# Performance work log

Hardware: AMD Instinct MI355X
Metric: run time of the kernel (lower is better)

Reference implementation:

```python
import jax, jax.numpy as jnp
import numpy as np

N_WIRES = 12
N_QLAYERS = 2
DIM = 2 ** N_WIRES


def setup_inputs() -> dict:
    key = jax.random.key(0)
    k0, k1, k2, k3 = jax.random.split(key, 4)
    x = jax.random.normal(k0, (2048, 1024), dtype=jnp.float32)
    # TT cores: ranks [1,16,1], input dims [32,32], output dims [8,9]
    core0 = jax.random.normal(k1, (1, 32, 8, 16), dtype=jnp.float32) * 0.05
    core1 = jax.random.normal(k2, (16, 32, 9, 1), dtype=jnp.float32) * 0.05
    tt_bias = jnp.zeros((72,), dtype=jnp.float32)
    global_angles = jax.random.normal(k3, (N_QLAYERS, N_WIRES, 3), dtype=jnp.float32) * 0.1
    return {"x": x, "core0": core0, "core1": core1, "tt_bias": tt_bias,
            "global_angles": global_angles}


def _rot(angles):
    # angles [..., 3] -> combined U = Rz @ Ry @ Rx, shape [..., 2, 2] complex64
    half = angles * 0.5
    cx, sx = jnp.cos(half[..., 0]), jnp.sin(half[..., 0])
    cy, sy = jnp.cos(half[..., 1]), jnp.sin(half[..., 1])
    cz, sz = jnp.cos(half[..., 2]), jnp.sin(half[..., 2])
    zero = jnp.zeros_like(cx)
    cplx = jax.lax.complex
    Rx = jnp.stack([jnp.stack([cplx(cx, zero), cplx(zero, -sx)], -1),
                    jnp.stack([cplx(zero, -sx), cplx(cx, zero)], -1)], -2)
    Ry = jnp.stack([jnp.stack([cplx(cy, zero), cplx(-sy, zero)], -1),
                    jnp.stack([cplx(sy, zero), cplx(cy, zero)], -1)], -2)
    ez, ezc = cplx(cz, -sz), cplx(cz, sz)  # exp(-i z/2), exp(+i z/2)
    zc = cplx(zero, zero)
    Rz = jnp.stack([jnp.stack([ez, zc], -1), jnp.stack([zc, ezc], -1)], -2)
    return jnp.einsum('...ij,...jk,...kl->...il', Rz, Ry, Rx)


def _apply_1q(state, U, w):
    # state [bsz, 2^n]; U [bsz, 2, 2]; wire 0 = most significant qubit
    bsz = state.shape[0]
    left, right = 2 ** w, 2 ** (N_WIRES - w - 1)
    s = state.reshape(bsz, left, 2, right)
    s = jnp.einsum('bij,bljr->blir', U, s)
    return s.reshape(bsz, DIM)


def _cnot(state, c, t):
    bsz = state.shape[0]
    s = state.reshape((bsz,) + (2,) * N_WIRES)
    s0 = jax.lax.index_in_dim(s, 0, c + 1, keepdims=True)
    s1 = jax.lax.index_in_dim(s, 1, c + 1, keepdims=True)
    s1 = jnp.flip(s1, axis=t + 1)  # flip target amplitudes where control = 1
    return jnp.concatenate([s0, s1], axis=c + 1).reshape(bsz, DIM)


def reference(x, core0, core1, tt_bias, global_angles):
    bsz = x.shape[0]
    # --- TT layer: x[b,32,32] contracted with two TT cores -> [b,8,9] -> [b,72]
    x_rs = x.reshape(bsz, 32, 32)
    tt_out = jnp.einsum('bij,aipq,qjrs->bpr', x_rs, core0, core1).reshape(bsz, -1) + tt_bias
    # residual global angles
    angles = global_angles[None, :, :, :] + tt_out.reshape(bsz, N_QLAYERS, N_WIRES, 3)
    U = _rot(angles)  # [bsz, L, n, 2, 2]
    # --- tensor-product Ry encoding of x[:, :n_wires] on |0...0>
    enc = x[:, :N_WIRES] * 0.5
    amp = jnp.stack([jnp.cos(enc), jnp.sin(enc)], -1)  # [bsz, n, 2]
    state = amp[:, 0, :]
    for w in range(1, N_WIRES):
        state = (state[:, :, None] * amp[:, w, None, :]).reshape(bsz, -1)
    state = state.astype(jnp.complex64)  # [bsz, 2^n]
    # --- VQC layers: fused Rz@Ry@Rx per wire, then ring CNOT (noise_prob=0)
    for k in range(N_QLAYERS):
        for w in range(N_WIRES):
            state = _apply_1q(state, U[:, k, w], w)
        for i in range(N_WIRES - 1):
            state = _cnot(state, i, i + 1)
        state = _cnot(state, N_WIRES - 1, 0)
    # --- MeasureAll(PauliZ): <Z_w> per wire
    probs = jnp.real(state * jnp.conj(state))  # [bsz, 2^n]
    idx = jnp.arange(DIM)[:, None]
    bits = (idx >> jnp.arange(N_WIRES - 1, -1, -1)[None, :]) & 1  # [2^n, n]
    zsign = (1.0 - 2.0 * bits).astype(jnp.float32)
    return probs @ zsign  # [bsz, n_wires]
```

## Files before the change

### kernel.cpp

```cpp
#include <hip/hip_runtime.h>
#include <math.h>

#define N_WIRES 12

__host__ __device__ constexpr int parity12(int x) {
  x ^= x >> 8; x ^= x >> 4; x ^= x >> 2; x ^= x >> 1;
  return x & 1;
}

typedef float2 f2;
__device__ __forceinline__ f2 mk2(float a, float b) { f2 r; r.x = a; r.y = b; return r; }
__device__ __forceinline__ f2 pkmul(f2 a, f2 b) {
  f2 d; asm("v_pk_mul_f32 %0, %1, %2" : "=v"(d) : "v"(a), "v"(b)); return d;
}
__device__ __forceinline__ f2 pkfma(f2 a, f2 b, f2 c) {
  f2 d; asm("v_pk_fma_f32 %0, %1, %2, %3" : "=v"(d) : "v"(a), "v"(b), "v"(c)); return d;
}
__device__ __forceinline__ f2 shfl_xor2(f2 v, int m) {
  f2 r; r.x = __shfl_xor(v.x, m, 64); r.y = __shfl_xor(v.y, m, 64); return r;
}
__device__ __forceinline__ f2 swap2(f2 v) { return mk2(v.y, v.x); }

__global__ __launch_bounds__(256) void build_w_kernel(
    const float* __restrict__ core0,
    const float* __restrict__ core1,
    float* __restrict__ Wt) {
  int idx = blockIdx.x * 256 + threadIdx.x;
  int k = idx / 72;
  int o = idx - k * 72;
  int i = k >> 5, jj = k & 31;
  int p = o / 9, r = o - p * 9;
  float acc = 0.f;
#pragma unroll
  for (int q = 0; q < 16; ++q) {
    acc += core0[(i * 8 + p) * 16 + q] * core1[(q * 32 + jj) * 9 + r];
  }
  int og = o / 9, j = o - og * 9;
  Wt[k * 96 + og * 12 + j] = acc;
}

__global__ __launch_bounds__(512) void tt_gemm2(
    const float* __restrict__ x,
    const float* __restrict__ Wt,
    const float* __restrict__ bias,
    float* __restrict__ ttout) {
  __shared__ __align__(16) float ws[128 * 96];
  __shared__ __align__(16) float xs[8 * 132];
  __shared__ float part[16 * 8 * 73];
  const int t = threadIdx.x;
  const int row0 = blockIdx.x * 8;
  const int kk = t >> 5;
  const int rp = (t >> 3) & 3;
  const int og = t & 7;
  const int r0 = rp * 2;

  float a0[9], a1[9];
#pragma unroll
  for (int j = 0; j < 9; ++j) { a0[j] = 0.f; a1[j] = 0.f; }

  for (int s = 0; s < 8; ++s) {
    __syncthreads();
    const float4* Wg = (const float4*)(Wt + s * 128 * 96);
#pragma unroll
    for (int i = 0; i < 6; ++i) {
      const int idx = i * 512 + t;
      ((float4*)ws)[idx] = Wg[idx];
    }
    if (t < 256) {
      const int rr = t >> 5, j4 = t & 31;
      *(float4*)&xs[rr * 132 + j4 * 4] =
          *(const float4*)(x + (size_t)(row0 + rr) * 1024 + s * 128 + j4 * 4);
    }
    __syncthreads();
#pragma unroll
    for (int i = 0; i < 8; ++i) {
      const int k = kk + i * 16;
      const float4 wA = *(const float4*)&ws[k * 96 + og * 12];
      const float4 wB = *(const float4*)&ws[k * 96 + og * 12 + 4];
      const float w8 = ws[k * 96 + og * 12 + 8];
      const float x0v = xs[r0 * 132 + k];
      const float x1v = xs[r0 * 132 + 132 + k];
      a0[0] += x0v * wA.x; a0[1] += x0v * wA.y;
      a0[2] += x0v * wA.z; a0[3] += x0v * wA.w;
      a0[4] += x0v * wB.x; a0[5] += x0v * wB.y;
      a0[6] += x0v * wB.z; a0[7] += x0v * wB.w;
      a0[8] += x0v * w8;
      a1[0] += x1v * wA.x; a1[1] += x1v * wA.y;
      a1[2] += x1v * wA.z; a1[3] += x1v * wA.w;
      a1[4] += x1v * wB.x; a1[5] += x1v * wB.y;
      a1[6] += x1v * wB.z; a1[7] += x1v * wB.w;
      a1[8] += x1v * w8;
    }
  }

#pragma unroll
  for (int j = 0; j < 9; ++j) {
    part[(kk * 8 + r0) * 73 + og * 9 + j] = a0[j];
    part[(kk * 8 + r0 + 1) * 73 + og * 9 + j] = a1[j];
  }
  __syncthreads();

  for (int i = t; i < 576; i += 512) {
    const int r = i / 72, o = i - r * 72;
    float ssum = bias[o];
#pragma unroll
    for (int kq = 0; kq < 16; ++kq) ssum += part[(kq * 8 + r) * 73 + o];
    ttout[(size_t)(row0 + r) * 72 + o] = ssum;
  }
}

template <int MASK, int ROW>
__device__ __forceinline__ void gate_pk(f2 R[8], f2 I[8],
    float u00r, float u00i, float u01r, float u01i,
    f2* __restrict__ buf, int t) {
  constexpr int RM = MASK & 15;
  constexpr int TM = (MASK >> 4) & 0xFF;
  constexpr int LM = TM & 63;
  constexpr bool LDSX = (TM & 0xC0) != 0;
  constexpr int FLIP = parity12(ROW & 3);
  constexpr int JX = (RM == 0) ? 0 : (((RM & 1) ? (RM ^ 3) : RM) >> 1);
  constexpr bool SW = (RM & 1) != 0;

  const int tsgn = (__popc(ROW & (t << 4)) & 1) << 31;
  const float dEi = __int_as_float(__float_as_int(u00i) ^ tsgn);
  const float oEr = __int_as_float(__float_as_int(u01r) ^ tsgn);
  const float ndEi = -dEi, noEr = -oEr;
  const f2 A  = mk2(u00r, u00r);
  const f2 C  = mk2(u01i, u01i);
  const f2 nC = mk2(-u01i, -u01i);

  auto Dof = [&](int pe, int ph) { return mk2(pe ? ndEi : dEi, ph ? ndEi : dEi); };
  auto Oof = [&](int pe, int ph) { return mk2(pe ? noEr : oEr, ph ? noEr : oEr); };

  auto upd = [&](int j, f2 Rb, f2 Ib, f2& outR, f2& outI) {
    const int pe = parity12(ROW & (2 * j));
    const int ph = pe ^ FLIP;
    const f2 Dj = Dof(pe, ph), nDj = Dof(!pe, !ph), Oj = Oof(pe, ph);
    const f2 a = R[j], ii = I[j];
    outR = pkfma(A, a, pkfma(nDj, ii, pkfma(Oj, Rb, pkmul(nC, Ib))));
    outI = pkfma(Dj, a, pkfma(A, ii, pkfma(C, Rb, pkmul(Oj, Ib))));
  };

  if constexpr (LDSX) {
    const int tp = t ^ TM;
#pragma unroll
    for (int ph2 = 0; ph2 < 2; ++ph2) {
      __syncthreads();
#pragma unroll
      for (int j = 0; j < 8; ++j) {
        const bool inA = (j < 2) || (j > 5);
        if ((ph2 == 0) == inA) {
          const int slot = inA ? ((j < 2) ? j : j - 4) : (j - 2);
          buf[slot * 512 + t] = R[j];
          buf[slot * 512 + 256 + t] = I[j];
        }
      }
      __syncthreads();
#pragma unroll
      for (int j = 0; j < 8; ++j) {
        const bool inA = (j < 2) || (j > 5);
        if ((ph2 == 0) == inA) {
          const int j2 = j ^ JX;
          const bool inA2 = (j2 < 2) || (j2 > 5);
          const int slot2 = inA2 ? ((j2 < 2) ? j2 : j2 - 4) : (j2 - 2);
          f2 Rb = buf[slot2 * 512 + tp];
          f2 Ib = buf[slot2 * 512 + 256 + tp];
          if constexpr (SW) { Rb = swap2(Rb); Ib = swap2(Ib); }
          upd(j, Rb, Ib, R[j], I[j]);
        }
      }
    }
  } else if constexpr (LM != 0) {
#pragma unroll
    for (int j = 0; j < 8; ++j) {
      const f2 Rb = shfl_xor2(R[j], LM);
      const f2 Ib = shfl_xor2(I[j], LM);
      upd(j, Rb, Ib, R[j], I[j]);
    }
  } else {
#pragma unroll
    for (int j = 0; j < 8; ++j) {
      const int j2 = j ^ JX;
      if (j < j2) {
        f2 Rb1 = R[j2], Ib1 = I[j2], Rb2 = R[j], Ib2 = I[j];
        if constexpr (SW) {
          Rb1 = swap2(Rb1); Ib1 = swap2(Ib1);
          Rb2 = swap2(Rb2); Ib2 = swap2(Ib2);
        }
        f2 nR1, nI1, nR2, nI2;
        upd(j, Rb1, Ib1, nR1, nI1);
        upd(j2, Rb2, Ib2, nR2, nI2);
        R[j] = nR1; I[j] = nI1; R[j2] = nR2; I[j2] = nI2;
      }
    }
  }
}

__global__ __launch_bounds__(256, 5) void vqc_kernel4(
    const float* __restrict__ x,
    const float* __restrict__ ttout,
    const float* __restrict__ gang,
    float* __restrict__ out) {
  const int b = blockIdx.x;
  const int t = threadIdx.x;

  __shared__ __align__(16) f2 buf[2048];
  __shared__ float sU[12][4];
  __shared__ float sFre[12][2], sFim[12][2];

  const float* ttb = ttout + (size_t)b * 72;

  if (t < 24) {
    const int w = (t < 12) ? t : t - 12;
    const int k = (t < 12) ? 1 : 0;
    const int gbase = (k * 12 + w) * 3;
    const int tbase = k * 36 + w * 3;
    float a0 = gang[gbase + 0] + ttb[tbase + 0];
    float a1 = gang[gbase + 1] + ttb[tbase + 1];
    float a2 = gang[gbase + 2] + ttb[tbase + 2];
    float cx = cosf(0.5f * a0), sx = sinf(0.5f * a0);
    float cy = cosf(0.5f * a1), sy = sinf(0.5f * a1);
    float cz = cosf(0.5f * a2), sz = sinf(0.5f * a2);
    float m00r = cy * cx,   m00i = sy * sx;
    float m01r = -sy * cx,  m01i = -cy * sx;
    float m10r = sy * cx,   m10i = -cy * sx;
    float m11r = cy * cx,   m11i = -sy * sx;
    float U00r = cz * m00r + sz * m00i, U00i = cz * m00i - sz * m00r;
    float U01r = cz * m01r + sz * m01i, U01i = cz * m01i - sz * m01r;
    float U10r = cz * m10r - sz * m10i, U10i = cz * m10i + sz * m10r;
    float U11r = cz * m11r - sz * m11i, U11i = cz * m11i + sz * m11r;
    if (t < 12) {
      sU[w][0] = U00r; sU[w][1] = U00i;
      sU[w][2] = U01r; sU[w][3] = U01i;
    } else {
      const float e = x[(size_t)b * 1024 + w] * 0.5f;
      const float c = cosf(e), s = sinf(e);
      sFre[w][0] = U00r * c + U01r * s;  sFim[w][0] = U00i * c + U01i * s;
      sFre[w][1] = U10r * c + U11r * s;  sFim[w][1] = U10i * c + U11i * s;
    }
  }
  __syncthreads();

  float vr[16], vi[16];
  {
    const int bits[7] = {(t >> 7) & 1,
                         ((t >> 6) ^ (t >> 5)) & 1,
                         ((t >> 5) ^ (t >> 4)) & 1,
                         ((t >> 4) ^ (t >> 3)) & 1,
                         ((t >> 3) ^ (t >> 2)) & 1,
                         ((t >> 2) ^ (t >> 1)) & 1,
                         ((t >> 1) ^ t) & 1};
    float br_ = 1.f, bi_ = 0.f;
#pragma unroll
    for (int w = 0; w < 7; ++w) {
      const float fr = sFre[w][bits[w]], fi = sFim[w][bits[w]];
      const float nr = br_ * fr - bi_ * fi;
      const float ni = br_ * fi + bi_ * fr;
      br_ = nr; bi_ = ni;
    }
    const int t0 = t & 1;
    float b7r[2], b7i[2];
#pragma unroll
    for (int r3 = 0; r3 < 2; ++r3) {
      const float fr = sFre[7][t0 ^ r3], fi = sFim[7][t0 ^ r3];
      b7r[r3] = br_ * fr - bi_ * fi;
      b7i[r3] = br_ * fi + bi_ * fr;
    }
    float hr[8], hi[8];
#pragma unroll
    for (int j = 0; j < 8; ++j) {
      const int r3 = j >> 2, r2 = (j >> 1) & 1, r1 = j & 1;
      const float ar = sFre[8][r3 ^ r2], ai = sFim[8][r3 ^ r2];
      const float cr = sFre[9][r2 ^ r1], ci = sFim[9][r2 ^ r1];
      hr[j] = ar * cr - ai * ci; hi[j] = ar * ci + ai * cr;
    }
    float gr[4], gi[4];
#pragma unroll
    for (int j = 0; j < 4; ++j) {
      const int r1 = j >> 1, r0 = j & 1;
      const float ar = sFre[10][r1 ^ r0], ai = sFim[10][r1 ^ r0];
      const float cr = sFre[11][r0], ci = sFim[11][r0];
      gr[j] = ar * cr - ai * ci; gi[j] = ar * ci + ai * cr;
    }
#pragma unroll
    for (int r = 0; r < 16; ++r) {
      const int r3 = r >> 3, hj = r >> 1, gj = r & 3;
      const float pr = hr[hj] * gr[gj] - hi[hj] * gi[gj];
      const float pi = hr[hj] * gi[gj] + hi[hj] * gr[gj];
      vr[r] = b7r[r3] * pr - b7i[r3] * pi;
      vi[r] = b7r[r3] * pi + b7i[r3] * pr;
    }
  }
  f2 R[8], I[8];
#pragma unroll
  for (int j = 0; j < 8; ++j) {
    R[j] = mk2(vr[2 * j], vr[(2 * j) ^ 3]);
    I[j] = mk2(vi[2 * j], vi[(2 * j) ^ 3]);
  }

#define GATE(MASK, ROW, GID) \
  gate_pk<MASK, ROW>(R, I, sU[GID][0], sU[GID][1], sU[GID][2], sU[GID][3], buf, t)

  GATE(0xC00, 0x400, 0);
  GATE(0x200, 0xE00, 1);
  GATE(0x100, 0xD00, 2);
  GATE(0x080, 0xC80, 3);
  GATE(0x040, 0xC40, 4);
  GATE(0x020, 0xC20, 5);
  GATE(0x010, 0xC10, 6);
  GATE(0x008, 0xC08, 7);
  GATE(0x004, 0xC04, 8);
  GATE(0x002, 0xC02, 9);
  GATE(0x001, 0xC01, 10);
  GATE(0xBFF, 0xC00, 11);
#undef GATE

  constexpr int MROWS[12] = {0xFFF, 0xA00, 0x700, 0xB80, 0x7C0, 0xBE0,
                             0x7F0, 0xBF8, 0x7FC, 0xBFE, 0x7FF, 0xBFF};
  const f2 Spp = mk2(1.f, 1.f),  Smm = mk2(-1.f, -1.f);
  const f2 Spm = mk2(1.f, -1.f), Smp = mk2(-1.f, 1.f);
  f2 acc2[12];
#pragma unroll
  for (int w = 0; w < 12; ++w) acc2[w] = mk2(0.f, 0.f);
#pragma unroll
  for (int j = 0; j < 8; ++j) {
    const f2 pr2 = pkfma(I[j], I[j], pkmul(R[j], R[j]));
#pragma unroll
    for (int w = 0; w < 12; ++w) {
      const int sl = parity12(MROWS[w] & (2 * j));
      const int sh = sl ^ parity12(MROWS[w] & 3);
      const f2 S = sl ? (sh ? Smm : Smp) : (sh ? Spm : Spp);
      acc2[w] = pkfma(S, pr2, acc2[w]);
    }
  }
  __syncthreads();
  float* rbuf = (float*)buf;
#pragma unroll
  for (int w = 0; w < 12; ++w) {
    float v = acc2[w].x + acc2[w].y;
    if (__popc(MROWS[w] & (t << 4)) & 1) v = -v;
#pragma unroll
    for (int off = 32; off > 0; off >>= 1) v += __shfl_down(v, off, 64);
    if ((t & 63) == 0) rbuf[(t >> 6) * 12 + w] = v;
  }
  __syncthreads();
  if (t < 12) {
    out[(size_t)b * 12 + t] = rbuf[t] + rbuf[12 + t] + rbuf[24 + t] + rbuf[36 + t];
  }
}

extern "C" void kernel_launch(void* const* d_in, const int* in_sizes, int n_in,
                              void* d_out, int out_size, void* d_ws, size_t ws_size,
                              hipStream_t stream) {
  const float* x       = (const float*)d_in[0];
  const float* core0   = (const float*)d_in[1];
  const float* core1   = (const float*)d_in[2];
  const float* tt_bias = (const float*)d_in[3];
  const float* gang    = (const float*)d_in[4];
  float* out = (float*)d_out;
  float* Wt     = (float*)d_ws;
  float* ttout  = (float*)d_ws + 98304;

  const int bsz = in_sizes[0] / 1024;

  build_w_kernel<<<288, 256, 0, stream>>>(core0, core1, Wt);
  tt_gemm2<<<bsz / 8, 512, 0, stream>>>(x, Wt, tt_bias, ttout);
  vqc_kernel4<<<bsz, 256, 0, stream>>>(x, ttout, gang, out);
}
```

Baseline: 58.79 us.

## Simulate each sample's statevector within a single wavefront to drop LDS exchanges

The VQC kernel now assigns one 64-lane wavefront per batch sample, with 64 amplitudes held in registers per lane (32 packed pairs), instead of one 256-thread block per sample with 16 per thread. Every gate is then done with register swaps or cross-lane shuffles, so the shared-memory exchange and __syncthreads barriers of high-wire gates go away. Unitary coefficients are broadcast with shuffles instead of LDS, and the final reduction writes straight from lane 0. The cost is about four times the register state per thread and lower occupancy (launch bounds changed from 5 to 2), plus more shuffles per gate, which risks spills and less latency hiding.

```diff
diff --git a/kernel.cpp b/kernel.cpp
--- a/kernel.cpp
+++ b/kernel.cpp
@@ -20,6 +20,11 @@
   f2 r; r.x = __shfl_xor(v.x, m, 64); r.y = __shfl_xor(v.y, m, 64); return r;
 }
 __device__ __forceinline__ f2 swap2(f2 v) { return mk2(v.y, v.x); }
+
+struct cpx { float r, i; };
+__device__ __forceinline__ cpx cmulc(cpx a, cpx b) {
+  return {a.r * b.r - a.i * b.i, a.r * b.i + a.i * b.r};
+}
 
 __global__ __launch_bounds__(256) void build_w_kernel(
     const float* __restrict__ core0,
@@ -110,18 +115,15 @@
 }
 
 template <int MASK, int ROW>
-__device__ __forceinline__ void gate_pk(f2 R[8], f2 I[8],
-    float u00r, float u00i, float u01r, float u01i,
-    f2* __restrict__ buf, int t) {
-  constexpr int RM = MASK & 15;
-  constexpr int TM = (MASK >> 4) & 0xFF;
-  constexpr int LM = TM & 63;
-  constexpr bool LDSX = (TM & 0xC0) != 0;
+__device__ __forceinline__ void gate_pk(f2 R[32], f2 I[32],
+    float u00r, float u00i, float u01r, float u01i, int lane) {
+  constexpr int RM = MASK & 0x3F;
+  constexpr int LM = (MASK >> 6) & 0x3F;
   constexpr int FLIP = parity12(ROW & 3);
   constexpr int JX = (RM == 0) ? 0 : (((RM & 1) ? (RM ^ 3) : RM) >> 1);
   constexpr bool SW = (RM & 1) != 0;
 
-  const int tsgn = (__popc(ROW & (t << 4)) & 1) << 31;
+  const int tsgn = (__popc((ROW >> 6) & lane) & 1) << 31;
   const float dEi = __int_as_float(__float_as_int(u00i) ^ tsgn);
   const float oEr = __int_as_float(__float_as_int(u01r) ^ tsgn);
   const float ndEi = -dEi, noEr = -oEr;
@@ -141,45 +143,35 @@
     outI = pkfma(Dj, a, pkfma(A, ii, pkfma(C, Rb, pkmul(Oj, Ib))));
   };
 
-  if constexpr (LDSX) {
-    const int tp = t ^ TM;
-#pragma unroll
-    for (int ph2 = 0; ph2 < 2; ++ph2) {
-      __syncthreads();
-#pragma unroll
-      for (int j = 0; j < 8; ++j) {
-        const bool inA = (j < 2) || (j > 5);
-        if ((ph2 == 0) == inA) {
-          const int slot = inA ? ((j < 2) ? j : j - 4) : (j - 2);
-          buf[slot * 512 + t] = R[j];
-          buf[slot * 512 + 256 + t] = I[j];
-        }
-      }
-      __syncthreads();
-#pragma unroll
-      for (int j = 0; j < 8; ++j) {
-        const bool inA = (j < 2) || (j > 5);
-        if ((ph2 == 0) == inA) {
-          const int j2 = j ^ JX;
-          const bool inA2 = (j2 < 2) || (j2 > 5);
-          const int slot2 = inA2 ? ((j2 < 2) ? j2 : j2 - 4) : (j2 - 2);
-          f2 Rb = buf[slot2 * 512 + tp];
-          f2 Ib = buf[slot2 * 512 + 256 + tp];
-          if constexpr (SW) { Rb = swap2(Rb); Ib = swap2(Ib); }
-          upd(j, Rb, Ib, R[j], I[j]);
-        }
-      }
-    }
-  } else if constexpr (LM != 0) {
-#pragma unroll
-    for (int j = 0; j < 8; ++j) {
+  if constexpr (LM != 0 && RM == 0) {
+#pragma unroll
+    for (int j = 0; j < 32; ++j) {
       const f2 Rb = shfl_xor2(R[j], LM);
       const f2 Ib = shfl_xor2(I[j], LM);
-      upd(j, Rb, Ib, R[j], I[j]);
+      f2 nR, nI;
+      upd(j, Rb, Ib, nR, nI);
+      R[j] = nR; I[j] = nI;
+    }
+  } else if constexpr (LM != 0 && RM != 0) {
+#pragma unroll
+    for (int j = 0; j < 32; ++j) {
+      const int j2 = j ^ JX;
+      if (j < j2) {
+        f2 Rb1 = shfl_xor2(R[j2], LM), Ib1 = shfl_xor2(I[j2], LM);
+        f2 Rb2 = shfl_xor2(R[j],  LM), Ib2 = shfl_xor2(I[j],  LM);
+        if constexpr (SW) {
+          Rb1 = swap2(Rb1); Ib1 = swap2(Ib1);
+          Rb2 = swap2(Rb2); Ib2 = swap2(Ib2);
+        }
+        f2 nR1, nI1, nR2, nI2;
+        upd(j, Rb1, Ib1, nR1, nI1);
+        upd(j2, Rb2, Ib2, nR2, nI2);
+        R[j] = nR1; I[j] = nI1; R[j2] = nR2; I[j2] = nI2;
+      }
     }
   } else {
 #pragma unroll
-    for (int j = 0; j < 8; ++j) {
+    for (int j = 0; j < 32; ++j) {
       const int j2 = j ^ JX;
       if (j < j2) {
         f2 Rb1 = R[j2], Ib1 = I[j2], Rb2 = R[j], Ib2 = I[j];
@@ -196,110 +188,121 @@
   }
 }
 
-__global__ __launch_bounds__(256, 5) void vqc_kernel4(
+__global__ __launch_bounds__(256, 2) void vqc_kernel5(
     const float* __restrict__ x,
     const float* __restrict__ ttout,
     const float* __restrict__ gang,
     float* __restrict__ out) {
-  const int b = blockIdx.x;
   const int t = threadIdx.x;
-
-  __shared__ __align__(16) f2 buf[2048];
-  __shared__ float sU[12][4];
-  __shared__ float sFre[12][2], sFim[12][2];
-
+  const int lane = t & 63;
+  const int b = blockIdx.x * 4 + (t >> 6);
   const float* ttb = ttout + (size_t)b * 72;
 
-  if (t < 24) {
-    const int w = (t < 12) ? t : t - 12;
-    const int k = (t < 12) ? 1 : 0;
+  float c0 = 0.f, c1 = 0.f, c2 = 0.f, c3 = 0.f;
+  const bool uLane = lane < 12;
+  const bool fLane = (lane >= 16) && (lane < 28);
+  if (uLane || fLane) {
+    const int w = uLane ? lane : lane - 16;
+    const int k = uLane ? 1 : 0;
     const int gbase = (k * 12 + w) * 3;
     const int tbase = k * 36 + w * 3;
-    float a0 = gang[gbase + 0] + ttb[tbase + 0];
-    float a1 = gang[gbase + 1] + ttb[tbase + 1];
-    float a2 = gang[gbase + 2] + ttb[tbase + 2];
-    float cx = cosf(0.5f * a0), sx = sinf(0.5f * a0);
-    float cy = cosf(0.5f * a1), sy = sinf(0.5f * a1);
-    float cz = cosf(0.5f * a2), sz = sinf(0.5f * a2);
-    float m00r = cy * cx,   m00i = sy * sx;
-    float m01r = -sy * cx,  m01i = -cy * sx;
-    float m10r = sy * cx,   m10i = -cy * sx;
-    float m11r = cy * cx,   m11i = -sy * sx;
-    float U00r = cz * m00r + sz * m00i, U00i = cz * m00i - sz * m00r;
-    float U01r = cz * m01r + sz * m01i, U01i = cz * m01i - sz * m01r;
-    float U10r = cz * m10r - sz * m10i, U10i = cz * m10i + sz * m10r;
-    float U11r = cz * m11r - sz * m11i, U11i = cz * m11i + sz * m11r;
-    if (t < 12) {
-      sU[w][0] = U00r; sU[w][1] = U00i;
-      sU[w][2] = U01r; sU[w][3] = U01i;
+    const float a0 = gang[gbase + 0] + ttb[tbase + 0];
+    const float a1 = gang[gbase + 1] + ttb[tbase + 1];
+    const float a2 = gang[gbase + 2] + ttb[tbase + 2];
+    const float cx = cosf(0.5f * a0), sx = sinf(0.5f * a0);
+    const float cy = cosf(0.5f * a1), sy = sinf(0.5f * a1);
+    const float cz = cosf(0.5f * a2), sz = sinf(0.5f * a2);
+    const float m00r = cy * cx,   m00i = sy * sx;
+    const float m01r = -sy * cx,  m01i = -cy * sx;
+    const float m10r = sy * cx,   m10i = -cy * sx;
+    const float m11r = cy * cx,   m11i = -sy * sx;
+    const float U00r = cz * m00r + sz * m00i, U00i = cz * m00i - sz * m00r;
+    const float U01r = cz * m01r + sz * m01i, U01i = cz * m01i - sz * m01r;
+    const float U10r = cz * m10r - sz * m10i, U10i = cz * m10i + sz * m10r;
+    const float U11r = cz * m11r - sz * m11i, U11i = cz * m11i + sz * m11r;
+    if (uLane) {
+      c0 = U00r; c1 = U00i; c2 = U01r; c3 = U01i;
     } else {
       const float e = x[(size_t)b * 1024 + w] * 0.5f;
-      const float c = cosf(e), s = sinf(e);
-      sFre[w][0] = U00r * c + U01r * s;  sFim[w][0] = U00i * c + U01i * s;
-      sFre[w][1] = U10r * c + U11r * s;  sFim[w][1] = U10i * c + U11i * s;
-    }
-  }
-  __syncthreads();
-
-  float vr[16], vi[16];
-  {
-    const int bits[7] = {(t >> 7) & 1,
-                         ((t >> 6) ^ (t >> 5)) & 1,
-                         ((t >> 5) ^ (t >> 4)) & 1,
-                         ((t >> 4) ^ (t >> 3)) & 1,
-                         ((t >> 3) ^ (t >> 2)) & 1,
-                         ((t >> 2) ^ (t >> 1)) & 1,
-                         ((t >> 1) ^ t) & 1};
-    float br_ = 1.f, bi_ = 0.f;
-#pragma unroll
-    for (int w = 0; w < 7; ++w) {
-      const float fr = sFre[w][bits[w]], fi = sFim[w][bits[w]];
-      const float nr = br_ * fr - bi_ * fi;
-      const float ni = br_ * fi + bi_ * fr;
-      br_ = nr; bi_ = ni;
-    }
-    const int t0 = t & 1;
-    float b7r[2], b7i[2];
-#pragma unroll
-    for (int r3 = 0; r3 < 2; ++r3) {
-      const float fr = sFre[7][t0 ^ r3], fi = sFim[7][t0 ^ r3];
-      b7r[r3] = br_ * fr - bi_ * fi;
-      b7i[r3] = br_ * fi + bi_ * fr;
-    }
-    float hr[8], hi[8];
-#pragma unroll
-    for (int j = 0; j < 8; ++j) {
-      const int r3 = j >> 2, r2 = (j >> 1) & 1, r1 = j & 1;
-      const float ar = sFre[8][r3 ^ r2], ai = sFim[8][r3 ^ r2];
-      const float cr = sFre[9][r2 ^ r1], ci = sFim[9][r2 ^ r1];
-      hr[j] = ar * cr - ai * ci; hi[j] = ar * ci + ai * cr;
-    }
-    float gr[4], gi[4];
-#pragma unroll
-    for (int j = 0; j < 4; ++j) {
-      const int r1 = j >> 1, r0 = j & 1;
-      const float ar = sFre[10][r1 ^ r0], ai = sFim[10][r1 ^ r0];
-      const float cr = sFre[11][r0], ci = sFim[11][r0];
-      gr[j] = ar * cr - ai * ci; gi[j] = ar * ci + ai * cr;
-    }
-#pragma unroll
-    for (int r = 0; r < 16; ++r) {
-      const int r3 = r >> 3, hj = r >> 1, gj = r & 3;
-      const float pr = hr[hj] * gr[gj] - hi[hj] * gi[gj];
-      const float pi = hr[hj] * gi[gj] + hi[hj] * gr[gj];
-      vr[r] = b7r[r3] * pr - b7i[r3] * pi;
-      vi[r] = b7r[r3] * pi + b7i[r3] * pr;
-    }
-  }
-  f2 R[8], I[8];
-#pragma unroll
-  for (int j = 0; j < 8; ++j) {
-    R[j] = mk2(vr[2 * j], vr[(2 * j) ^ 3]);
-    I[j] = mk2(vi[2 * j], vi[(2 * j) ^ 3]);
-  }
-
-#define GATE(MASK, ROW, GID) \
-  gate_pk<MASK, ROW>(R, I, sU[GID][0], sU[GID][1], sU[GID][2], sU[GID][3], buf, t)
+      const float cc = cosf(e), ss = sinf(e);
+      c0 = U00r * cc + U01r * ss;  c1 = U00i * cc + U01i * ss;
+      c2 = U10r * cc + U11r * ss;  c3 = U10i * cc + U11i * ss;
+    }
+  }
+
+  float Fr[12][2], Fi[12][2];
+#pragma unroll
+  for (int w = 0; w < 12; ++w) {
+    Fr[w][0] = __shfl(c0, 16 + w, 64);
+    Fi[w][0] = __shfl(c1, 16 + w, 64);
+    Fr[w][1] = __shfl(c2, 16 + w, 64);
+    Fi[w][1] = __shfl(c3, 16 + w, 64);
+  }
+
+  const int bw0 = (lane >> 5) & 1;
+  const int bw1 = ((lane >> 4) ^ (lane >> 3)) & 1;
+  const int bw2 = ((lane >> 3) ^ (lane >> 2)) & 1;
+  const int bw3 = ((lane >> 2) ^ (lane >> 1)) & 1;
+  const int bw4 = ((lane >> 1) ^ lane) & 1;
+  const int l0 = lane & 1;
+
+  cpx P = {bw0 ? Fr[0][1] : Fr[0][0], bw0 ? Fi[0][1] : Fi[0][0]};
+  P = cmulc(P, {bw1 ? Fr[1][1] : Fr[1][0], bw1 ? Fi[1][1] : Fi[1][0]});
+  P = cmulc(P, {bw2 ? Fr[2][1] : Fr[2][0], bw2 ? Fi[2][1] : Fi[2][0]});
+  P = cmulc(P, {bw3 ? Fr[3][1] : Fr[3][0], bw3 ? Fi[3][1] : Fi[3][0]});
+  P = cmulc(P, {bw4 ? Fr[4][1] : Fr[4][0], bw4 ? Fi[4][1] : Fi[4][0]});
+
+  cpx A1[2];
+  A1[0] = {l0 ? Fr[5][1] : Fr[5][0], l0 ? Fi[5][1] : Fi[5][0]};
+  A1[1] = {l0 ? Fr[5][0] : Fr[5][1], l0 ? Fi[5][0] : Fi[5][1]};
+  cpx A2[4];
+#pragma unroll
+  for (int a = 0; a < 2; ++a)
+#pragma unroll
+    for (int bb = 0; bb < 2; ++bb)
+      A2[a * 2 + bb] = cmulc(A1[a], {Fr[6][a ^ bb], Fi[6][a ^ bb]});
+  cpx A3[8];
+#pragma unroll
+  for (int i = 0; i < 4; ++i)
+#pragma unroll
+    for (int bb = 0; bb < 2; ++bb)
+      A3[i * 2 + bb] = cmulc(A2[i], {Fr[7][(i & 1) ^ bb], Fi[7][(i & 1) ^ bb]});
+  cpx A4[16];
+#pragma unroll
+  for (int i = 0; i < 8; ++i)
+#pragma unroll
+    for (int bb = 0; bb < 2; ++bb)
+      A4[i * 2 + bb] = cmulc(A3[i], {Fr[8][(i & 1) ^ bb], Fi[8][(i & 1) ^ bb]});
+
+  cpx T2[4];
+#pragma unroll
+  for (int j = 0; j < 4; ++j)
+    T2[j] = cmulc({Fr[10][(j >> 1) ^ (j & 1)], Fi[10][(j >> 1) ^ (j & 1)]},
+                  {Fr[11][j & 1], Fi[11][j & 1]});
+  cpx TP[8];
+#pragma unroll
+  for (int r2 = 0; r2 < 2; ++r2)
+#pragma unroll
+    for (int j = 0; j < 4; ++j)
+      TP[r2 * 4 + j] = cmulc(P,
+          cmulc({Fr[9][r2 ^ (j >> 1)], Fi[9][r2 ^ (j >> 1)]}, T2[j]));
+
+  f2 R[32], I[32];
+#pragma unroll
+  for (int j = 0; j < 32; ++j) {
+    const cpx Av = A4[j >> 1];
+    const int lo = (((j >> 1) & 1) << 2) | ((j & 1) << 1);
+    const int hi = (((j >> 1) & 1) << 2) | (((j & 1) ^ 1) << 1) | 1;
+    const f2 Tre = mk2(TP[lo].r, TP[hi].r);
+    const f2 Tim = mk2(TP[lo].i, TP[hi].i);
+    const f2 Ar = mk2(Av.r, Av.r);
+    R[j] = pkfma(mk2(-Av.i, -Av.i), Tim, pkmul(Ar, Tre));
+    I[j] = pkfma(mk2(Av.i, Av.i), Tre, pkmul(Ar, Tim));
+  }
+
+#define GATE(MASK, ROW, G)                                                  \
+  gate_pk<MASK, ROW>(R, I, __shfl(c0, G, 64), __shfl(c1, G, 64),            \
+                     __shfl(c2, G, 64), __shfl(c3, G, 64), lane)
 
   GATE(0xC00, 0x400, 0);
   GATE(0x200, 0xE00, 1);
@@ -323,7 +326,7 @@
 #pragma unroll
   for (int w = 0; w < 12; ++w) acc2[w] = mk2(0.f, 0.f);
 #pragma unroll
-  for (int j = 0; j < 8; ++j) {
+  for (int j = 0; j < 32; ++j) {
     const f2 pr2 = pkfma(I[j], I[j], pkmul(R[j], R[j]));
 #pragma unroll
     for (int w = 0; w < 12; ++w) {
@@ -333,19 +336,13 @@
       acc2[w] = pkfma(S, pr2, acc2[w]);
     }
   }
-  __syncthreads();
-  float* rbuf = (float*)buf;
 #pragma unroll
   for (int w = 0; w < 12; ++w) {
     float v = acc2[w].x + acc2[w].y;
-    if (__popc(MROWS[w] & (t << 4)) & 1) v = -v;
+    if (__popc((MROWS[w] >> 6) & lane) & 1) v = -v;
 #pragma unroll
     for (int off = 32; off > 0; off >>= 1) v += __shfl_down(v, off, 64);
-    if ((t & 63) == 0) rbuf[(t >> 6) * 12 + w] = v;
-  }
-  __syncthreads();
-  if (t < 12) {
-    out[(size_t)b * 12 + t] = rbuf[t] + rbuf[12 + t] + rbuf[24 + t] + rbuf[36 + t];
+    if (lane == 0) out[(size_t)b * 12 + w] = v;
   }
 }
 
@@ -365,5 +362,5 @@
 
   build_w_kernel<<<288, 256, 0, stream>>>(core0, core1, Wt);
   tt_gemm2<<<bsz / 8, 512, 0, stream>>>(x, Wt, tt_bias, ttout);
-  vqc_kernel4<<<bsz, 256, 0, stream>>>(x, ttout, gang, out);
-}
+  vqc_kernel5<<<bsz / 4, 256, 0, stream>>>(x, ttout, gang, out);
+}
```

New measurement: 54.61 us. 1.08x faster.
